# Optimization experiments

Hardware: AMD Instinct MI355X
Metric: run time of the kernel (lower is better)

## Reference

```python
import jax, jax.numpy as jnp
import numpy as np

N, E, F_IN, H, C = 50000, 800000, 256, 4, 32
NEG_SLOPE_ATT = 0.2   # PyG GATConv default negative_slope for attention LeakyReLU
NEG_SLOPE_ACT = 0.01  # GATLayer's alpha for the post-norm LeakyReLU
EPS = 1e-5            # BatchNorm1d eps


def setup_inputs() -> dict:
    key = jax.random.key(0)
    ks = jax.random.split(key, 8)
    x = jax.random.normal(ks[0], (N, F_IN), jnp.float32)
    edge_idx = jax.random.randint(ks[1], (2, E), 0, N)
    # GATConv params (heads concatenated): lin weight, attention vectors, bias
    W = jax.random.normal(ks[2], (H * C, F_IN), jnp.float32) / np.sqrt(F_IN)
    att_src = jax.random.normal(ks[3], (H, C), jnp.float32) / np.sqrt(C)
    att_dst = jax.random.normal(ks[4], (H, C), jnp.float32) / np.sqrt(C)
    bias = jax.random.normal(ks[5], (H * C,), jnp.float32) * 0.01
    # BatchNorm1d affine params
    gamma = jax.random.normal(ks[6], (H * C,), jnp.float32) * 0.1 + 1.0
    beta = jax.random.normal(ks[7], (H * C,), jnp.float32) * 0.01
    return {"x": x, "edge_idx": edge_idx, "W": W, "att_src": att_src,
            "att_dst": att_dst, "bias": bias, "gamma": gamma, "beta": beta}


def reference(x, edge_idx, W, att_src, att_dst, bias, gamma, beta):
    n = x.shape[0]
    # PyG GATConv adds self-loops by default
    self_loops = jnp.arange(n)
    src = jnp.concatenate([edge_idx[0], self_loops])  # [E+N]
    dst = jnp.concatenate([edge_idx[1], self_loops])

    h = (x @ W.T).reshape(n, H, C)                    # [N, H, C]
    a_s = jnp.einsum('nhc,hc->nh', h, att_src)        # per-node src score
    a_d = jnp.einsum('nhc,hc->nh', h, att_dst)        # per-node dst score

    # edge attention logits, then segment softmax over incoming edges per dst
    e = jax.nn.leaky_relu(a_s[src] + a_d[dst], NEG_SLOPE_ATT)  # [E+N, H]
    e_max = jax.ops.segment_max(e, dst, num_segments=n)
    e_exp = jnp.exp(e - e_max[dst])
    denom = jax.ops.segment_sum(e_exp, dst, num_segments=n)
    alpha = e_exp / denom[dst]                        # [E+N, H]

    # scatter-add aggregation of attended source features
    out = jax.ops.segment_sum(alpha[:, :, None] * h[src], dst, num_segments=n)
    out = out.reshape(n, H * C) + bias                # concat heads + bias

    # BatchNorm1d (training-mode batch statistics) + LeakyReLU(alpha)
    mu = out.mean(axis=0)
    var = out.var(axis=0)
    out = (out - mu) * jax.lax.rsqrt(var + EPS) * gamma + beta
    return jax.nn.leaky_relu(out, NEG_SLOPE_ACT)
```

## Files before the change

kernel.cpp:

```cpp
#include <hip/hip_runtime.h>
#include <hip/hip_bf16.h>
#include <hip/hip_fp16.h>
#include <math.h>


typedef __attribute__((ext_vector_type(8))) short bf8_t;
typedef __attribute__((ext_vector_type(4))) float f4_t;

__device__ inline unsigned short f2bf(float f) {
  unsigned u = __float_as_uint(f);
  u += 0x7fff + ((u >> 16) & 1);
  return (unsigned short)(u >> 16);
}
__device__ inline unsigned cvtpk(float a, float b) {
  unsigned r;
  asm("v_cvt_pk_bf16_f32 %0, %1, %2" : "=v"(r) : "v"(a), "v"(b));
  return r;
}
__device__ inline unsigned cvtpk_f16(float a, float b) {
  unsigned r;
  asm("v_cvt_pkrtz_f16_f32 %0, %1, %2" : "=v"(r) : "v"(a), "v"(b));
  return r;
}
__device__ inline float lrelu02(float v) { return v > 0.f ? v : 0.2f * v; }
__device__ inline float f16lo(unsigned g) {
  return __half2float(__ushort_as_half((unsigned short)(g & 0xffffu)));
}
__device__ inline float f16hi(unsigned g) {
  return __half2float(__ushort_as_half((unsigned short)(g >> 16)));
}

#define LSTRIDE 264
#define PSTRIDE 2048
#define SSTRIDE 2112
#define NC 32

__global__ __launch_bounds__(256) void att_fold_k(const float* __restrict__ w,
                                                  const float* __restrict__ att_s,
                                                  const float* __restrict__ att_d,
                                                  float* __restrict__ waug) {
  int j = blockIdx.x;
  int head = j & 3;
  const float* av = (j < 4 ? att_s : att_d) + head * 32;
  int col = threadIdx.x;
  float s = 0.f;
#pragma unroll
  for (int c = 0; c < 32; c++)
    s += av[c] * w[(size_t)(head * 32 + c) * 256 + col];
  waug[j * 256 + col] = s;
}

__global__ __launch_bounds__(256) void gemm_mfma(const float* __restrict__ x,
                                                 const float* __restrict__ w,
                                                 const float* __restrict__ waug,
                                                 unsigned* __restrict__ hb2,
                                                 float* __restrict__ a_s,
                                                 float* __restrict__ a_d,
                                                 int n, int ntiles) {
  __shared__ unsigned short wsl[144 * LSTRIDE];
  __shared__ unsigned short xsl[64 * LSTRIDE];
  int tid = threadIdx.x;
  int lane = tid & 63;
  int wid = tid >> 6;
  int quad = lane >> 4;
  int l15 = lane & 15;

#pragma unroll 4
  for (int i = 0; i < 32; i++) {
    int idx = tid + i * 256;
    int row = idx >> 6;
    int f4 = idx & 63;
    float4 v = *(const float4*)&w[(size_t)row * 256 + f4 * 4];
    *(uint2*)&wsl[row * LSTRIDE + f4 * 4] =
        make_uint2(cvtpk(v.x, v.y), cvtpk(v.z, v.w));
  }
#pragma unroll
  for (int i = 0; i < 8; i++) {
    int idx = tid + i * 256;
    int row = idx >> 8;
    int col = idx & 255;
    float v = waug[idx];
    unsigned short hi = f2bf(v);
    float lov = v - __uint_as_float((unsigned)hi << 16);
    wsl[(128 + row) * LSTRIDE + col] = hi;
    wsl[(136 + row) * LSTRIDE + col] = f2bf(lov);
  }

  float4 pre[16];
  int tile = blockIdx.x;
  if (tile < ntiles) {
#pragma unroll
    for (int i = 0; i < 16; i++) {
      int idx = tid + i * 256;
      int row = idx >> 6, f4 = idx & 63;
      int grow = tile * 64 + row;
      pre[i] = (grow < n) ? *(const float4*)&x[(size_t)grow * 256 + f4 * 4]
                          : make_float4(0.f, 0.f, 0.f, 0.f);
    }
  }

  for (; tile < ntiles; tile += gridDim.x) {
    __syncthreads();
#pragma unroll
    for (int i = 0; i < 16; i++) {
      int idx = tid + i * 256;
      int row = idx >> 6, f4 = idx & 63;
      *(uint2*)&xsl[row * LSTRIDE + f4 * 4] =
          make_uint2(cvtpk(pre[i].x, pre[i].y), cvtpk(pre[i].z, pre[i].w));
    }
    __syncthreads();

    int nxt = tile + gridDim.x;
    if (nxt < ntiles) {
#pragma unroll
      for (int i = 0; i < 16; i++) {
        int idx = tid + i * 256;
        int row = idx >> 6, f4 = idx & 63;
        int grow = nxt * 64 + row;
        pre[i] = (grow < n) ? *(const float4*)&x[(size_t)grow * 256 + f4 * 4]
                            : make_float4(0.f, 0.f, 0.f, 0.f);
      }
    }

    f4_t acc[9];
#pragma unroll
    for (int t = 0; t < 9; t++) acc[t] = (f4_t){0.f, 0.f, 0.f, 0.f};
    const unsigned short* arow = &xsl[(wid * 16 + l15) * LSTRIDE];
#pragma unroll
    for (int ks = 0; ks < 8; ks++) {
      bf8_t af = *(const bf8_t*)&arow[ks * 32 + quad * 8];
#pragma unroll
      for (int t = 0; t < 9; t++) {
        bf8_t bf = *(const bf8_t*)&wsl[(t * 16 + l15) * LSTRIDE + ks * 32 + quad * 8];
        acc[t] = __builtin_amdgcn_mfma_f32_16x16x32_bf16(af, bf, acc[t], 0, 0, 0);
      }
    }

    int growb = tile * 64 + wid * 16 + quad * 4;
#pragma unroll
    for (int r = 0; r < 4; r++) {
      int grow = growb + r;
      bool ok = grow < n;
      if (ok) {
        unsigned* orow = &hb2[(size_t)grow * 64];
#pragma unroll
        for (int t = 0; t < 4; t++)
          orow[t * 16 + l15] = cvtpk_f16(acc[t][r], acc[t + 4][r]);
      }
      float v8 = acc[8][r];
      v8 += __shfl_xor(v8, 8, 64);
      if (ok) {
        if (l15 < 4) a_s[grow * 4 + l15] = v8;
        else if (l15 < 8) a_d[grow * 4 + (l15 - 4)] = v8;
      }
    }
  }
}

__global__ __launch_bounds__(1024) void pair_scatter3_k(const int* __restrict__ src,
                                                        const int* __restrict__ dst,
                                                        int* __restrict__ bcnt,
                                                        unsigned* __restrict__ pairs,
                                                        int E, int nb) {
  __shared__ int cnt[1024];
  int t = threadIdx.x;
  int chunk = (E + gridDim.x - 1) / gridDim.x;
  int lo = blockIdx.x * chunk;
  int hi = min(E, lo + chunk);
  for (int i = t; i < nb; i += 1024) cnt[i] = 0;
  __syncthreads();
  for (int i = lo + t; i < hi; i += 1024) atomicAdd(&cnt[dst[i] >> 6], 1);
  __syncthreads();
  for (int i = t; i < nb; i += 1024) {
    int c = cnt[i];
    cnt[i] = c ? atomicAdd(&bcnt[i], c) : 0;
  }
  __syncthreads();
  for (int i = lo + t; i < hi; i += 1024) {
    int d = dst[i];
    int b = d >> 6;
    int pos = atomicAdd(&cnt[b], 1);
    if (pos < PSTRIDE)
      pairs[(size_t)b * PSTRIDE + pos] = (unsigned)src[i] | ((unsigned)(d & 63) << 26);
  }
}

__global__ __launch_bounds__(256) void bucket_csr_k(const unsigned* __restrict__ pairs,
                                                    const int* __restrict__ bcnt,
                                                    int* __restrict__ off,
                                                    int* __restrict__ dlen,
                                                    int* __restrict__ ssrc, int n) {
  __shared__ int hist[64], lofs[64], curs[64];
  int b = blockIdx.x;
  int t = threadIdx.x;
  int d0 = b << 6;
  int dcnt = min(64, n - d0);
  int cnt = min(bcnt[b], PSTRIDE);
  size_t pstart = (size_t)b * PSTRIDE;
  int ob = b * SSTRIDE;
  if (t < 64) hist[t] = (t < dcnt) ? 1 : 0;
  __syncthreads();
  for (int i = t; i < cnt; i += 256) atomicAdd(&hist[pairs[pstart + i] >> 26], 1);
  __syncthreads();
  if (t == 0) {
    int acc = 0;
    for (int k = 0; k < 64; k++) { lofs[k] = acc; acc += hist[k]; }
  }
  __syncthreads();
  if (t < dcnt) {
    int lo = lofs[t];
    off[d0 + t] = ob + lo;
    dlen[d0 + t] = hist[t];
    curs[t] = lo + 1;
    ssrc[ob + lo] = d0 + t;
  }
  __syncthreads();
  for (int i = t; i < cnt; i += 256) {
    unsigned u = pairs[pstart + i];
    int dl = u >> 26;
    int pos = ob + atomicAdd(&curs[dl], 1);
    ssrc[pos] = (int)(u & 0x03FFFFFFu);
  }
}

#define FMA4(g, p)                                                            \
  alo0 = fmaf(f16lo(g.x), p.x, alo0); ahi0 = fmaf(f16hi(g.x), p.y, ahi0);     \
  alo1 = fmaf(f16lo(g.y), p.x, alo1); ahi1 = fmaf(f16hi(g.y), p.y, ahi1);     \
  alo2 = fmaf(f16lo(g.z), p.x, alo2); ahi2 = fmaf(f16hi(g.z), p.y, ahi2);     \
  alo3 = fmaf(f16lo(g.w), p.x, alo3); ahi3 = fmaf(f16hi(g.w), p.y, ahi3);     \
  dlo += p.x; dhi += p.y;

__global__ __launch_bounds__(256) void agg_csr_k(const int* __restrict__ off,
                                                 const int* __restrict__ dlen,
                                                 const int* __restrict__ ssrc,
                                                 const float* __restrict__ a_s,
                                                 const float* __restrict__ a_d,
                                                 const unsigned* __restrict__ hb2,
                                                 float* __restrict__ out,
                                                 float* __restrict__ gstat, int n) {
  __shared__ float lp[4][64 * 4];
  __shared__ float bstat[4][256];
  int tid = threadIdx.x;
  int wid = tid >> 6;
  int lane = tid & 63;
  int q = lane >> 4;
  int m = lane & 15;
  int hsel = m >> 3;
  unsigned mo = (unsigned)m * 4u;

  int d = blockIdx.x * 4 + wid;
  bool act = d < n;

  float alo0 = 0.f, alo1 = 0.f, alo2 = 0.f, alo3 = 0.f;
  float ahi0 = 0.f, ahi1 = 0.f, ahi2 = 0.f, ahi3 = 0.f;
  float dlo = 0.f, dhi = 0.f;

  if (act) {
    int start = off[d];
    int end = start + dlen[d];
    float4 ad4 = *(const float4*)&a_d[(unsigned)d * 4u];
    for (int base = start; base < end; base += 64) {
      int cnt = min(64, end - base);
      int j = base + lane;
      int s = ssrc[(unsigned)min(j, end - 1)];

      uint4 g0, g1;
      bool pipe = (cnt >= 8);
      if (pipe) {
        unsigned s0 = (unsigned)__shfl(s, q, 64);
        unsigned s1 = (unsigned)__shfl(s, 4 + q, 64);
        g0 = *(const uint4*)&hb2[s0 * 64u + mo];
        g1 = *(const uint4*)&hb2[s1 * 64u + mo];
      }

      float4 as4 = *(const float4*)&a_s[(unsigned)s * 4u];
      float p0 = __expf(lrelu02(as4.x + ad4.x));
      float p1 = __expf(lrelu02(as4.y + ad4.y));
      float p2 = __expf(lrelu02(as4.z + ad4.z));
      float p3 = __expf(lrelu02(as4.w + ad4.w));
      *(float4*)&lp[wid][lane * 4] = make_float4(p0, p2, p1, p3);

      int k = 0;
      for (; k + 16 <= cnt; k += 8) {
        unsigned s0n = (unsigned)__shfl(s, k + 8 + q, 64);
        unsigned s1n = (unsigned)__shfl(s, k + 12 + q, 64);
        uint4 h0 = *(const uint4*)&hb2[s0n * 64u + mo];
        uint4 h1 = *(const uint4*)&hb2[s1n * 64u + mo];
        float2 pp0 = *(const float2*)&lp[wid][(k + q) * 4 + hsel * 2];
        float2 pp1 = *(const float2*)&lp[wid][(k + 4 + q) * 4 + hsel * 2];
        FMA4(g0, pp0);
        FMA4(g1, pp1);
        g0 = h0; g1 = h1;
      }
      if (pipe) {
        float2 pp0 = *(const float2*)&lp[wid][(k + q) * 4 + hsel * 2];
        float2 pp1 = *(const float2*)&lp[wid][(k + 4 + q) * 4 + hsel * 2];
        FMA4(g0, pp0);
        FMA4(g1, pp1);
        k += 8;
      }
      for (; k + 4 <= cnt; k += 4) {
        unsigned s0 = (unsigned)__shfl(s, k + q, 64);
        uint4 g = *(const uint4*)&hb2[s0 * 64u + mo];
        float2 pp = *(const float2*)&lp[wid][(k + q) * 4 + hsel * 2];
        FMA4(g, pp);
      }
      int rem = cnt - k;
      if (rem > 0) {
        int e = min(k + q, cnt - 1);
        unsigned s0 = (unsigned)__shfl(s, e, 64);
        uint4 g = *(const uint4*)&hb2[s0 * 64u + mo];
        float2 pp = *(const float2*)&lp[wid][e * 4 + hsel * 2];
        if (q < rem) { FMA4(g, pp); }
      }
    }
  }

#pragma unroll
  for (int o = 16; o < 64; o <<= 1) {
    alo0 += __shfl_xor(alo0, o, 64); alo1 += __shfl_xor(alo1, o, 64);
    alo2 += __shfl_xor(alo2, o, 64); alo3 += __shfl_xor(alo3, o, 64);
    ahi0 += __shfl_xor(ahi0, o, 64); ahi1 += __shfl_xor(ahi1, o, 64);
    ahi2 += __shfl_xor(ahi2, o, 64); ahi3 += __shfl_xor(ahi3, o, 64);
    dlo += __shfl_xor(dlo, o, 64);   dhi += __shfl_xor(dhi, o, 64);
  }
  float il_lo = 1.0f / dlo;
  float il_hi = 1.0f / dhi;
  float4 flo = make_float4(0.f, 0.f, 0.f, 0.f);
  float4 fhi = make_float4(0.f, 0.f, 0.f, 0.f);
  if (act) {
    flo = make_float4(alo0 * il_lo, alo1 * il_lo, alo2 * il_lo, alo3 * il_lo);
    fhi = make_float4(ahi0 * il_hi, ahi1 * il_hi, ahi2 * il_hi, ahi3 * il_hi);
  }
  if (q == 0) {
    if (act) {
      *(float4*)&out[(unsigned)d * 128u + m * 4] = flo;
      *(float4*)&out[(unsigned)d * 128u + 64 + m * 4] = fhi;
    }
    *(float4*)&bstat[wid][m * 4] = flo;
    *(float4*)&bstat[wid][64 + m * 4] = fhi;
    *(float4*)&bstat[wid][128 + m * 4] =
        make_float4(flo.x * flo.x, flo.y * flo.y, flo.z * flo.z, flo.w * flo.w);
    *(float4*)&bstat[wid][192 + m * 4] =
        make_float4(fhi.x * fhi.x, fhi.y * fhi.y, fhi.z * fhi.z, fhi.w * fhi.w);
  }
  __syncthreads();
  float v = bstat[0][tid] + bstat[1][tid] + bstat[2][tid] + bstat[3][tid];
  atomicAdd(&gstat[(blockIdx.x & (NC - 1)) * 256 + tid], v);
}

__global__ __launch_bounds__(128) void bn_coef_k(const float* __restrict__ gstat,
                                                 const float* __restrict__ gamma,
                                                 const float* __restrict__ beta,
                                                 float* __restrict__ coef,
                                                 float inv_n) {
  int tid = threadIdx.x;
  float s = 0.f, s2 = 0.f;
#pragma unroll 8
  for (int c = 0; c < NC; c++) {
    s += gstat[c * 256 + tid];
    s2 += gstat[c * 256 + 128 + tid];
  }
  float mu = s * inv_n;
  float var = s2 * inv_n - mu * mu;
  float rstd = 1.0f / sqrtf(var + 1e-5f);
  float g = gamma[tid] * rstd;
  coef[tid] = g;
  coef[128 + tid] = beta[tid] - mu * g;
}

__global__ __launch_bounds__(256) void bn_apply_k(float* __restrict__ out,
                                                  const float* __restrict__ coef,
                                                  int n4) {
  __shared__ float sc[128], sh[128];
  int tid = threadIdx.x;
  if (tid < 128) {
    sc[tid] = coef[tid];
    sh[tid] = coef[128 + tid];
  }
  __syncthreads();
  int i = blockIdx.x * 256 + tid;
  if (i >= n4) return;
  float4 v = ((float4*)out)[i];
  int j = (i & 31) << 2;
  const float4 scv = *(const float4*)&sc[j];
  const float4 shv = *(const float4*)&sh[j];
  v.x = fmaf(v.x, scv.x, shv.x);
  v.y = fmaf(v.y, scv.y, shv.y);
  v.z = fmaf(v.z, scv.z, shv.z);
  v.w = fmaf(v.w, scv.w, shv.w);
  v.x = v.x > 0.f ? v.x : 0.01f * v.x;
  v.y = v.y > 0.f ? v.y : 0.01f * v.y;
  v.z = v.z > 0.f ? v.z : 0.01f * v.z;
  v.w = v.w > 0.f ? v.w : 0.01f * v.w;
  ((float4*)out)[i] = v;
}

static inline char* align16(char* p) {
  return (char*)(((uintptr_t)p + 15) & ~(uintptr_t)15);
}

extern "C" void kernel_launch(void* const* d_in, const int* in_sizes, int n_in,
                              void* d_out, int out_size, void* d_ws, size_t ws_size,
                              hipStream_t stream) {
  const float* x     = (const float*)d_in[0];
  const int*   ei    = (const int*)d_in[1];
  const float* W     = (const float*)d_in[2];
  const float* att_s = (const float*)d_in[3];
  const float* att_d = (const float*)d_in[4];
  const float* gamma = (const float*)d_in[6];
  const float* beta  = (const float*)d_in[7];

  int n = in_sizes[0] / 256;
  int E = in_sizes[1] / 2;
  const int* src = ei;
  const int* dstp = ei + E;
  float* out = (float*)d_out;

  int NBUCK = (n + 63) >> 6;
  int ntiles = (n + 63) / 64;

  char* p = (char*)d_ws;
  unsigned* hb2 = (unsigned*)p; p = align16(p + (size_t)n * 64 * 4);
  float* a_s   = (float*)p; p = align16(p + (size_t)n * 4 * 4);
  float* a_d   = (float*)p; p = align16(p + (size_t)n * 4 * 4);
  float* waug  = (float*)p; p = align16(p + 8 * 256 * 4);
  float* gstat = (float*)p;
  float* coef  = gstat + NC * 256;
  int*   bcnt  = (int*)(coef + 256);
  p = align16((char*)(bcnt + NBUCK));
  int* off     = (int*)p;   p = align16(p + (size_t)n * 4);
  int* dlen    = (int*)p;   p = align16(p + (size_t)n * 4);
  int* ssrc    = (int*)p;   p = align16(p + (size_t)NBUCK * SSTRIDE * 4);
  unsigned* pairs = (unsigned*)p; p = align16(p + (size_t)NBUCK * PSTRIDE * 4);

  hipMemsetAsync(gstat, 0, ((size_t)NC * 256 + 256 + NBUCK) * 4, stream);

  att_fold_k<<<8, 256, 0, stream>>>(W, att_s, att_d, waug);
  gemm_mfma<<<256, 256, 0, stream>>>(x, W, waug, hb2, a_s, a_d, n, ntiles);

  pair_scatter3_k<<<256, 1024, 0, stream>>>(src, dstp, bcnt, pairs, E, NBUCK);
  bucket_csr_k<<<NBUCK, 256, 0, stream>>>(pairs, bcnt, off, dlen, ssrc, n);

  agg_csr_k<<<(n + 3) / 4, 256, 0, stream>>>(off, dlen, ssrc, a_s, a_d, hb2, out,
                                             gstat, n);

  bn_coef_k<<<1, 128, 0, stream>>>(gstat, gamma, beta, coef, 1.0f / n);
  bn_apply_k<<<(n * 32 + 255) / 256, 256, 0, stream>>>(out, coef, n * 32);
}
```

Baseline: 193.2 us.

## Fold att-vector kernel and BN coef kernel into neighbors, load A directly

Removes the att_fold and bn_coef launches. The attention-folded weight rows are now computed inside every GEMM block, and the BN coefficients are recomputed by every bn_apply block from fewer stat copies (NC 32→8). The GEMM also drops the LDS staging and register prefetch for x: each lane loads its A fragment directly from global memory and converts it to bf16. The grid doubles to 512 blocks so occupancy hides the latency. This trades two launches and LDS traffic for redundant per-block work and more atomic contention on the 8 stat slots.

New measurement: 203.8 us. 1.05x slower.

```diff
diff --git a/kernel.cpp b/kernel.cpp
--- a/kernel.cpp
+++ b/kernel.cpp
@@ -33,32 +33,17 @@
 #define LSTRIDE 264
 #define PSTRIDE 2048
 #define SSTRIDE 2112
-#define NC 32
-
-__global__ __launch_bounds__(256) void att_fold_k(const float* __restrict__ w,
-                                                  const float* __restrict__ att_s,
-                                                  const float* __restrict__ att_d,
-                                                  float* __restrict__ waug) {
-  int j = blockIdx.x;
-  int head = j & 3;
-  const float* av = (j < 4 ? att_s : att_d) + head * 32;
-  int col = threadIdx.x;
-  float s = 0.f;
-#pragma unroll
-  for (int c = 0; c < 32; c++)
-    s += av[c] * w[(size_t)(head * 32 + c) * 256 + col];
-  waug[j * 256 + col] = s;
-}
+#define NC 8
 
 __global__ __launch_bounds__(256) void gemm_mfma(const float* __restrict__ x,
                                                  const float* __restrict__ w,
-                                                 const float* __restrict__ waug,
+                                                 const float* __restrict__ att_s,
+                                                 const float* __restrict__ att_d,
                                                  unsigned* __restrict__ hb2,
                                                  float* __restrict__ a_s,
                                                  float* __restrict__ a_d,
                                                  int n, int ntiles) {
   __shared__ unsigned short wsl[144 * LSTRIDE];
-  __shared__ unsigned short xsl[64 * LSTRIDE];
   int tid = threadIdx.x;
   int lane = tid & 63;
   int wid = tid >> 6;
@@ -74,65 +59,53 @@
     *(uint2*)&wsl[row * LSTRIDE + f4 * 4] =
         make_uint2(cvtpk(v.x, v.y), cvtpk(v.z, v.w));
   }
-#pragma unroll
-  for (int i = 0; i < 8; i++) {
-    int idx = tid + i * 256;
-    int row = idx >> 8;
-    int col = idx & 255;
-    float v = waug[idx];
-    unsigned short hi = f2bf(v);
-    float lov = v - __uint_as_float((unsigned)hi << 16);
-    wsl[(128 + row) * LSTRIDE + col] = hi;
-    wsl[(136 + row) * LSTRIDE + col] = f2bf(lov);
-  }
-
-  float4 pre[16];
-  int tile = blockIdx.x;
-  if (tile < ntiles) {
-#pragma unroll
-    for (int i = 0; i < 16; i++) {
-      int idx = tid + i * 256;
-      int row = idx >> 6, f4 = idx & 63;
-      int grow = tile * 64 + row;
-      pre[i] = (grow < n) ? *(const float4*)&x[(size_t)grow * 256 + f4 * 4]
-                          : make_float4(0.f, 0.f, 0.f, 0.f);
-    }
-  }
-
-  for (; tile < ntiles; tile += gridDim.x) {
-    __syncthreads();
-#pragma unroll
-    for (int i = 0; i < 16; i++) {
-      int idx = tid + i * 256;
-      int row = idx >> 6, f4 = idx & 63;
-      *(uint2*)&xsl[row * LSTRIDE + f4 * 4] =
-          make_uint2(cvtpk(pre[i].x, pre[i].y), cvtpk(pre[i].z, pre[i].w));
-    }
-    __syncthreads();
-
-    int nxt = tile + gridDim.x;
-    if (nxt < ntiles) {
-#pragma unroll
-      for (int i = 0; i < 16; i++) {
-        int idx = tid + i * 256;
-        int row = idx >> 6, f4 = idx & 63;
-        int grow = nxt * 64 + row;
-        pre[i] = (grow < n) ? *(const float4*)&x[(size_t)grow * 256 + f4 * 4]
-                            : make_float4(0.f, 0.f, 0.f, 0.f);
-      }
+  {
+    int col = tid;
+#pragma unroll
+    for (int j = 0; j < 8; j++) {
+      int head = j & 3;
+      const float* av = (j < 4 ? att_s : att_d) + head * 32;
+      float s = 0.f;
+#pragma unroll
+      for (int c = 0; c < 32; c++)
+        s += av[c] * w[(size_t)(head * 32 + c) * 256 + col];
+      unsigned short hi = f2bf(s);
+      float lov = s - __uint_as_float((unsigned)hi << 16);
+      wsl[(128 + j) * LSTRIDE + col] = hi;
+      wsl[(136 + j) * LSTRIDE + col] = f2bf(lov);
+    }
+  }
+  __syncthreads();
+
+  int rowg = wid * 16 + l15;
+  int colb = quad * 8;
+  for (int tile = blockIdx.x; tile < ntiles; tile += gridDim.x) {
+    int garow = tile * 64 + rowg;
+    bf8_t a[8];
+    if (garow < n) {
+      const float* xr = &x[(size_t)garow * 256 + colb];
+#pragma unroll
+      for (int ks = 0; ks < 8; ks++) {
+        float4 v0 = *(const float4*)&xr[ks * 32];
+        float4 v1 = *(const float4*)&xr[ks * 32 + 4];
+        uint4 au = make_uint4(cvtpk(v0.x, v0.y), cvtpk(v0.z, v0.w),
+                              cvtpk(v1.x, v1.y), cvtpk(v1.z, v1.w));
+        a[ks] = *(bf8_t*)&au;
+      }
+    } else {
+#pragma unroll
+      for (int ks = 0; ks < 8; ks++) a[ks] = (bf8_t){0, 0, 0, 0, 0, 0, 0, 0};
     }
 
     f4_t acc[9];
 #pragma unroll
     for (int t = 0; t < 9; t++) acc[t] = (f4_t){0.f, 0.f, 0.f, 0.f};
-    const unsigned short* arow = &xsl[(wid * 16 + l15) * LSTRIDE];
 #pragma unroll
     for (int ks = 0; ks < 8; ks++) {
-      bf8_t af = *(const bf8_t*)&arow[ks * 32 + quad * 8];
 #pragma unroll
       for (int t = 0; t < 9; t++) {
         bf8_t bf = *(const bf8_t*)&wsl[(t * 16 + l15) * LSTRIDE + ks * 32 + quad * 8];
-        acc[t] = __builtin_amdgcn_mfma_f32_16x16x32_bf16(af, bf, acc[t], 0, 0, 0);
+        acc[t] = __builtin_amdgcn_mfma_f32_16x16x32_bf16(a[ks], bf, acc[t], 0, 0, 0);
       }
     }
 
@@ -349,34 +322,26 @@
   atomicAdd(&gstat[(blockIdx.x & (NC - 1)) * 256 + tid], v);
 }
 
-__global__ __launch_bounds__(128) void bn_coef_k(const float* __restrict__ gstat,
-                                                 const float* __restrict__ gamma,
-                                                 const float* __restrict__ beta,
-                                                 float* __restrict__ coef,
-                                                 float inv_n) {
-  int tid = threadIdx.x;
-  float s = 0.f, s2 = 0.f;
-#pragma unroll 8
-  for (int c = 0; c < NC; c++) {
-    s += gstat[c * 256 + tid];
-    s2 += gstat[c * 256 + 128 + tid];
-  }
-  float mu = s * inv_n;
-  float var = s2 * inv_n - mu * mu;
-  float rstd = 1.0f / sqrtf(var + 1e-5f);
-  float g = gamma[tid] * rstd;
-  coef[tid] = g;
-  coef[128 + tid] = beta[tid] - mu * g;
-}
-
 __global__ __launch_bounds__(256) void bn_apply_k(float* __restrict__ out,
-                                                  const float* __restrict__ coef,
-                                                  int n4) {
+                                                  const float* __restrict__ gstat,
+                                                  const float* __restrict__ gamma,
+                                                  const float* __restrict__ beta,
+                                                  float inv_n, int n4) {
   __shared__ float sc[128], sh[128];
   int tid = threadIdx.x;
   if (tid < 128) {
-    sc[tid] = coef[tid];
-    sh[tid] = coef[128 + tid];
+    float s = 0.f, s2 = 0.f;
+#pragma unroll
+    for (int c = 0; c < NC; c++) {
+      s += gstat[c * 256 + tid];
+      s2 += gstat[c * 256 + 128 + tid];
+    }
+    float mu = s * inv_n;
+    float var = s2 * inv_n - mu * mu;
+    float rstd = 1.0f / sqrtf(var + 1e-5f);
+    float g = gamma[tid] * rstd;
+    sc[tid] = g;
+    sh[tid] = beta[tid] - mu * g;
   }
   __syncthreads();
   int i = blockIdx.x * 256 + tid;
@@ -424,20 +389,17 @@
   unsigned* hb2 = (unsigned*)p; p = align16(p + (size_t)n * 64 * 4);
   float* a_s   = (float*)p; p = align16(p + (size_t)n * 4 * 4);
   float* a_d   = (float*)p; p = align16(p + (size_t)n * 4 * 4);
-  float* waug  = (float*)p; p = align16(p + 8 * 256 * 4);
   float* gstat = (float*)p;
-  float* coef  = gstat + NC * 256;
-  int*   bcnt  = (int*)(coef + 256);
+  int*   bcnt  = (int*)(gstat + NC * 256);
   p = align16((char*)(bcnt + NBUCK));
   int* off     = (int*)p;   p = align16(p + (size_t)n * 4);
   int* dlen    = (int*)p;   p = align16(p + (size_t)n * 4);
   int* ssrc    = (int*)p;   p = align16(p + (size_t)NBUCK * SSTRIDE * 4);
   unsigned* pairs = (unsigned*)p; p = align16(p + (size_t)NBUCK * PSTRIDE * 4);
 
-  hipMemsetAsync(gstat, 0, ((size_t)NC * 256 + 256 + NBUCK) * 4, stream);
-
-  att_fold_k<<<8, 256, 0, stream>>>(W, att_s, att_d, waug);
-  gemm_mfma<<<256, 256, 0, stream>>>(x, W, waug, hb2, a_s, a_d, n, ntiles);
+  hipMemsetAsync(gstat, 0, ((size_t)NC * 256 + NBUCK) * 4, stream);
+
+  gemm_mfma<<<512, 256, 0, stream>>>(x, W, att_s, att_d, hb2, a_s, a_d, n, ntiles);
 
   pair_scatter3_k<<<256, 1024, 0, stream>>>(src, dstp, bcnt, pairs, E, NBUCK);
   bucket_csr_k<<<NBUCK, 256, 0, stream>>>(pairs, bcnt, off, dlen, ssrc, n);
@@ -445,6 +407,6 @@
   agg_csr_k<<<(n + 3) / 4, 256, 0, stream>>>(off, dlen, ssrc, a_s, a_d, hb2, out,
                                              gstat, n);
 
-  bn_coef_k<<<1, 128, 0, stream>>>(gstat, gamma, beta, coef, 1.0f / n);
-  bn_apply_k<<<(n * 32 + 255) / 256, 256, 0, stream>>>(out, coef, n * 32);
-}
+  bn_apply_k<<<(n * 32 + 255) / 256, 256, 0, stream>>>(out, gstat, gamma, beta,
+                                                       1.0f / n, n * 32);
+}
```
